# Optimization experiments

Hardware: AMD Instinct MI355X
Metric: run time of the kernel (lower is better)

## Reference

```python
import jax, jax.numpy as jnp
import numpy as np

B, S, D = 2, 2048, 1024
H = 16
DH = D // H  # 64


def setup_inputs() -> dict:
    key = jax.random.key(0)
    k1, k2, k3 = jax.random.split(key, 3)
    X = jax.random.normal(k1, (B, S, D), dtype=jnp.float32)
    # xavier_normal for Linear(D, 3*D): std = sqrt(2/(fan_in+fan_out))
    std_qkv = float(np.sqrt(2.0 / (D + 3 * D)))
    std_out = float(np.sqrt(2.0 / (D + D)))
    W_qkv = jax.random.normal(k2, (3 * H * DH, D), dtype=jnp.float32) * std_qkv
    W_out = jax.random.normal(k3, (D, H * DH), dtype=jnp.float32) * std_out
    return {"X": X, "W_qkv": W_qkv, "W_out": W_out}


def reference(X, W_qkv, W_out):
    b, s, d = X.shape
    # stacked projection: (b, s, 3*H*DH), then per-head chunk into q,k,v
    qkv = jnp.einsum('bsd,ed->bse', X, W_qkv)
    qkv = qkv.reshape(b, s, H, 3 * DH)
    q, k, v = jnp.split(qkv, 3, axis=-1)  # each (b, s, H, DH)
    scale = 1.0 / jnp.sqrt(jnp.asarray(DH, dtype=X.dtype))
    # naive unfused attention: full [b,H,s,s] score matrix
    scores = jnp.einsum('bqhd,bkhd->bhqk', q, k) * scale
    attn = jax.nn.softmax(scores, axis=-1)
    vals = jnp.einsum('bhqk,bkhd->bqhd', attn, v)
    vals = vals.reshape(b, s, H * DH)
    out = jnp.einsum('bse,de->bsd', vals, W_out)
    return out
```

## Files before the change

### kernel.cpp

```cpp
#include <hip/hip_runtime.h>
#include <cstdint>
#include <cstddef>

typedef __bf16 bf16;
typedef __bf16 bf16x8 __attribute__((ext_vector_type(8)));
typedef __bf16 bf16x2 __attribute__((ext_vector_type(2)));
typedef float  floatx4 __attribute__((ext_vector_type(4)));

typedef __attribute__((address_space(1))) void gvoid_t;
typedef __attribute__((address_space(3))) void lvoid_t;

#define MFMA16(a, b, c) __builtin_amdgcn_mfma_f32_16x16x32_bf16((a), (b), (c), 0, 0, 0)

#if __has_builtin(__builtin_amdgcn_exp2f)
#define EXP2(x) __builtin_amdgcn_exp2f(x)
#else
#define EXP2(x) exp2f(x)
#endif

#define S_TOK 2048
#define E3 3072
#define DMODEL 1024

#define NX 4194304
#define NWQ 3145728
#define NWO 1048576
__global__ __launch_bounds__(256) void cvt_all(const float* __restrict__ X,
                                               const float* __restrict__ Wq,
                                               const float* __restrict__ Wo,
                                               bf16* __restrict__ Xb,
                                               bf16* __restrict__ Wqb,
                                               bf16* __restrict__ Wob) {
  int i = (blockIdx.x * 256 + threadIdx.x) * 8;
  const float* s;
  bf16* d;
  float sc = 1.0f;
  int off;
  if (i < NX) {
    s = X; d = Xb; off = i;
  } else if (i < NX + NWQ) {
    off = i - NX; s = Wq; d = Wqb;
    int row = off >> 10;
    if ((row % 192) < 64) sc = 0.18033688011f;
  } else {
    off = i - NX - NWQ; s = Wo; d = Wob;
  }
  const float4* p = (const float4*)(s + off);
  float4 a = p[0], b = p[1];
  bf16x8 o;
  o[0] = (bf16)(a.x * sc); o[1] = (bf16)(a.y * sc);
  o[2] = (bf16)(a.z * sc); o[3] = (bf16)(a.w * sc);
  o[4] = (bf16)(b.x * sc); o[5] = (bf16)(b.y * sc);
  o[6] = (bf16)(b.z * sc); o[7] = (bf16)(b.w * sc);
  *(bf16x8*)(d + off) = o;
}

__device__ __forceinline__ void gl_lds16(const bf16* g, bf16* l) {
  __builtin_amdgcn_global_load_lds((gvoid_t*)g, (lvoid_t*)l, 16, 0, 0);
}

template <bool OUT_BF16>
__global__ __launch_bounds__(256) void gemm_bt(const bf16* __restrict__ A,
                                               const bf16* __restrict__ Bt,
                                               void* __restrict__ Cv,
                                               int M, int N, int K) {
  __shared__ bf16 sA[128 * 64];
  __shared__ bf16 sB[128 * 64];
  const int tid = threadIdx.x;
  const int wv = tid >> 6, lane = tid & 63;
  const int wr = wv >> 1, wc = wv & 1;
  const int lrow = lane & 15, lgrp = lane >> 4;
  const int R0 = blockIdx.y * 128, C0 = blockIdx.x * 128;

  floatx4 acc[4][4] = {};

  const int srow = lane >> 3;
  const int schk = (lane & 7) ^ srow;
  const bf16* gA = A + (size_t)(R0 + wv * 32 + srow) * K + schk * 8;
  const bf16* gB = Bt + (size_t)(C0 + wv * 32 + srow) * K + schk * 8;
  bf16* lA = sA + wv * 32 * 64;
  bf16* lB = sB + wv * 32 * 64;
  const size_t rs8 = (size_t)8 * K;

  for (int k0 = 0; k0 < K; k0 += 64) {
#pragma unroll
    for (int c = 0; c < 4; c++) {
      gl_lds16(gA + k0 + c * rs8, lA + c * 512);
      gl_lds16(gB + k0 + c * rs8, lB + c * 512);
    }
    __syncthreads();
#pragma unroll
    for (int kk = 0; kk < 2; kk++) {
      bf16x8 af[4], bfr[4];
#pragma unroll
      for (int i = 0; i < 4; i++) {
        int r = wr * 64 + i * 16 + lrow;
        af[i] = *(const bf16x8*)&sA[r * 64 + ((kk * 4 + lgrp) ^ (r & 7)) * 8];
      }
#pragma unroll
      for (int j = 0; j < 4; j++) {
        int r = wc * 64 + j * 16 + lrow;
        bfr[j] = *(const bf16x8*)&sB[r * 64 + ((kk * 4 + lgrp) ^ (r & 7)) * 8];
      }
#pragma unroll
      for (int i = 0; i < 4; i++)
#pragma unroll
        for (int j = 0; j < 4; j++)
          acc[i][j] = MFMA16(af[i], bfr[j], acc[i][j]);
    }
    __syncthreads();
  }

  const int rbase = R0 + wr * 64 + lgrp * 4;
  const int cbase = C0 + wc * 64 + lrow;
  if (OUT_BF16) {
    bf16* C = (bf16*)Cv;
#pragma unroll
    for (int i = 0; i < 4; i++)
#pragma unroll
      for (int j = 0; j < 4; j++)
#pragma unroll
        for (int r = 0; r < 4; r++)
          C[(size_t)(rbase + i * 16 + r) * N + cbase + j * 16] = (bf16)acc[i][j][r];
  } else {
    float* C = (float*)Cv;
#pragma unroll
    for (int i = 0; i < 4; i++)
#pragma unroll
      for (int j = 0; j < 4; j++)
#pragma unroll
        for (int r = 0; r < 4; r++)
          C[(size_t)(rbase + i * 16 + r) * N + cbase + j * 16] = acc[i][j][r];
  }
}

__global__ __launch_bounds__(256) void transpose_v(const bf16* __restrict__ qkv,
                                                   bf16* __restrict__ Vt) {
  __shared__ bf16 sT[64 * 72];
  const int tid = threadIdx.x;
  const int b = blockIdx.z, h = blockIdx.y, s0 = blockIdx.x * 64;
  const bf16* vsrc = qkv + (size_t)(b * S_TOK + s0) * E3 + h * 192 + 128;
#pragma unroll
  for (int j = 0; j < 8; j++) {
    int idx = tid + 256 * j;
    int sl = idx & 63, dp = idx >> 6;
    unsigned u = *(const unsigned*)(vsrc + (size_t)sl * E3 + 2 * dp);
    sT[(2 * dp) * 72 + sl] = __builtin_bit_cast(bf16, (unsigned short)(u & 0xffffu));
    sT[(2 * dp + 1) * 72 + sl] = __builtin_bit_cast(bf16, (unsigned short)(u >> 16));
  }
  __syncthreads();
  bf16* vdst = Vt + ((size_t)(b * 16 + h) * 64) * S_TOK + s0;
#pragma unroll
  for (int j = 0; j < 2; j++) {
    int idx = tid + 256 * j;
    int d = idx >> 3, sc8 = (idx & 7) * 8;
    bf16x8 o;
#pragma unroll
    for (int m2 = 0; m2 < 8; m2++) {
      int sp = sc8 + m2;
      int ss = (sp & ~31) | ((sp >> 1) & 15) | ((sp & 1) << 4);
      o[m2] = sT[d * 72 + ss];
    }
    *(bf16x8*)(vdst + (size_t)d * S_TOK + sc8) = o;
  }
}

__global__ __launch_bounds__(256, 3) void attn(const bf16* __restrict__ qkv,
                                               const bf16* __restrict__ Vt,
                                               bf16* __restrict__ vals) {
  __shared__ bf16 sK[2][64 * 64];
  __shared__ bf16 sV[2][64 * 64];
  __shared__ bf16 sP[4][2][16 * 40];

  const int tid = threadIdx.x;
  const int wv = tid >> 6, lane = tid & 63;
  const int lrow = lane & 15, lgrp = lane >> 4;
  const int b = blockIdx.z, h = blockIdx.y;
  const int qb = blockIdx.x * 128;

  const int srow = lane >> 3;
  const int scol = (lane & 7) ^ srow;
  const bf16* kg0 = qkv + (size_t)(b * S_TOK + wv * 16 + srow) * E3 + h * 192 + 64 + scol * 8;
  const bf16* vg0 = Vt + (size_t)((b * 16 + h) * 64 + wv * 16 + srow) * S_TOK + scol * 8;

  const bf16* qp = qkv + (size_t)(b * S_TOK + qb + wv * 32) * E3 + h * 192;
  bf16x8 qa[2][2];
#pragma unroll
  for (int rt = 0; rt < 2; rt++)
#pragma unroll
    for (int dh = 0; dh < 2; dh++)
      qa[rt][dh] = *(const bf16x8*)(qp + (size_t)(rt * 16 + lrow) * E3 + dh * 32 + lgrp * 8);

  floatx4 O[2][4] = {};
  floatx4 lacc[2] = {};
  bf16x8 ones;
  const bf16 one1 = (bf16)1.0f;
#pragma unroll
  for (int j = 0; j < 8; j++) ones[j] = one1;

  const int xsw = (lrow & 7);

  auto stage = [&](int buf, int kt) {
    const bf16* kg = kg0 + (size_t)kt * 64 * E3;
    gl_lds16(kg, &sK[buf][wv * 1024]);
    gl_lds16(kg + (size_t)8 * E3, &sK[buf][wv * 1024 + 512]);
    const bf16* vg = vg0 + kt * 64;
    gl_lds16(vg, &sV[buf][wv * 1024]);
    gl_lds16(vg + 8 * S_TOK, &sV[buf][wv * 1024 + 512]);
  };

  auto compute = [&](int buf) {
#pragma unroll
    for (int g = 0; g < 2; g++) {
      bf16x8 kf[2][2];
#pragma unroll
      for (int t = 0; t < 2; t++)
#pragma unroll
        for (int dh = 0; dh < 2; dh++)
          kf[t][dh] = *(const bf16x8*)&sK[buf][(g * 32 + t * 16 + lrow) * 64 +
                                              ((dh * 4 + lgrp) ^ xsw) * 8];
#pragma unroll
      for (int rt = 0; rt < 2; rt++) {
        floatx4 sc0 = {0.f, 0.f, 0.f, 0.f}, sc1 = {0.f, 0.f, 0.f, 0.f};
        sc0 = MFMA16(qa[rt][0], kf[0][0], sc0);
        sc0 = MFMA16(qa[rt][1], kf[0][1], sc0);
        sc1 = MFMA16(qa[rt][0], kf[1][0], sc1);
        sc1 = MFMA16(qa[rt][1], kf[1][1], sc1);
#pragma unroll
        for (int r = 0; r < 4; r++) {
          bf16x2 h2;
          h2[0] = (bf16)EXP2(sc0[r]);
          h2[1] = (bf16)EXP2(sc1[r]);
          *(unsigned*)&sP[wv][rt][(lgrp * 4 + r) * 40 + lrow * 2] =
              __builtin_bit_cast(unsigned, h2);
        }
      }
      bf16x8 vf[4];
#pragma unroll
      for (int dt = 0; dt < 4; dt++)
        vf[dt] = *(const bf16x8*)&sV[buf][(dt * 16 + lrow) * 64 +
                                          ((g * 4 + lgrp) ^ xsw) * 8];
#pragma unroll
      for (int rt = 0; rt < 2; rt++) {
        bf16x8 pf = *(const bf16x8*)&sP[wv][rt][lrow * 40 + lgrp * 8];
#pragma unroll
        for (int dt = 0; dt < 4; dt++) O[rt][dt] = MFMA16(pf, vf[dt], O[rt][dt]);
        lacc[rt] = MFMA16(pf, ones, lacc[rt]);
      }
    }
  };

  stage(0, 0);
  __syncthreads();
#pragma unroll 1
  for (int kt = 0; kt < 32; kt += 2) {
    stage(1, kt + 1);
    compute(0);
    __syncthreads();
    if (kt + 2 < 32) stage(0, kt + 2);
    compute(1);
    __syncthreads();
  }

  bf16* vout = vals + (size_t)(b * S_TOK + qb + wv * 32) * DMODEL + h * 64;
#pragma unroll
  for (int rt = 0; rt < 2; rt++)
#pragma unroll
    for (int r = 0; r < 4; r++) {
      float rinv = __builtin_amdgcn_rcpf(lacc[rt][r]);
#pragma unroll
      for (int dt = 0; dt < 4; dt++)
        vout[(size_t)(rt * 16 + lgrp * 4 + r) * DMODEL + dt * 16 + lrow] =
            (bf16)(O[rt][dt][r] * rinv);
    }
}

extern "C" void kernel_launch(void* const* d_in, const int* in_sizes, int n_in,
                              void* d_out, int out_size, void* d_ws, size_t ws_size,
                              hipStream_t stream) {
  const float* X = (const float*)d_in[0];
  const float* Wqkv = (const float*)d_in[1];
  const float* Wout = (const float*)d_in[2];
  float* out = (float*)d_out;

  char* ws = (char*)d_ws;
  bf16* Xb = (bf16*)(ws);
  bf16* Wqb = (bf16*)(ws + ((size_t)8 << 20));
  bf16* Wob = (bf16*)(ws + ((size_t)14 << 20));
  bf16* qkvb = (bf16*)(ws + ((size_t)16 << 20));
  bf16* Vt = (bf16*)(ws + ((size_t)40 << 20));
  bf16* vals = (bf16*)(ws + ((size_t)48 << 20));

  cvt_all<<<(NX + NWQ + NWO) / 2048, 256, 0, stream>>>(X, Wqkv, Wout, Xb, Wqb, Wob);

  gemm_bt<true><<<dim3(24, 32), 256, 0, stream>>>(Xb, Wqb, qkvb, 4096, 3072, 1024);

  transpose_v<<<dim3(32, 16, 2), 256, 0, stream>>>(qkvb, Vt);

  attn<<<dim3(16, 16, 2), 256, 0, stream>>>(qkvb, Vt, vals);

  gemm_bt<false><<<dim3(8, 32), 256, 0, stream>>>(vals, Wob, out, 4096, 1024, 1024);
}
```

Before: 186.9 us.

## Fuse V transpose into QKV GEMM epilogue, widen attention blocks, narrow output GEMM tiles

The QKV GEMM epilogue now writes the V columns straight into the transposed, permuted Vt layout, which removes the separate transpose_v kernel and its round trip through global memory. The attention kernel moves to 512 threads, with each wave handling 16 query rows instead of 32, which cuts per-wave registers and raises waves per block. The output projection gets a new 128x64-tile GEMM that launches twice as many blocks so the device is better filled. The cost is scattered 2-byte stores in the fused epilogue and less reuse of K/V data per wave in attention.

```diff
diff --git a/kernel.cpp b/kernel.cpp
--- a/kernel.cpp
+++ b/kernel.cpp
@@ -59,10 +59,11 @@
   __builtin_amdgcn_global_load_lds((gvoid_t*)g, (lvoid_t*)l, 16, 0, 0);
 }
 
-template <bool OUT_BF16>
+template <bool OUT_BF16, bool FUSE_V>
 __global__ __launch_bounds__(256) void gemm_bt(const bf16* __restrict__ A,
                                                const bf16* __restrict__ Bt,
                                                void* __restrict__ Cv,
+                                               bf16* __restrict__ Vt,
                                                int M, int N, int K) {
   __shared__ bf16 sA[128 * 64];
   __shared__ bf16 sB[128 * 64];
@@ -118,10 +119,25 @@
 #pragma unroll
     for (int i = 0; i < 4; i++)
 #pragma unroll
-      for (int j = 0; j < 4; j++)
-#pragma unroll
-        for (int r = 0; r < 4; r++)
-          C[(size_t)(rbase + i * 16 + r) * N + cbase + j * 16] = (bf16)acc[i][j][r];
+      for (int j = 0; j < 4; j++) {
+        const int col = cbase + j * 16;
+        const int m192 = col % 192;
+        const int hh = col / 192;
+#pragma unroll
+        for (int r = 0; r < 4; r++) {
+          const int row = rbase + i * 16 + r;
+          bf16 val = (bf16)acc[i][j][r];
+          bf16* dst;
+          if (FUSE_V && m192 >= 128) {
+            const int sl = row & 2047;
+            const int sp = (sl & ~31) | ((sl & 15) << 1) | ((sl >> 4) & 1);
+            dst = Vt + ((size_t)(((row >> 11) * 16 + hh) * 64 + (m192 - 128))) * S_TOK + sp;
+          } else {
+            dst = C + (size_t)row * N + col;
+          }
+          *dst = val;
+        }
+      }
   } else {
     float* C = (float*)Cv;
 #pragma unroll
@@ -134,43 +150,73 @@
   }
 }
 
-__global__ __launch_bounds__(256) void transpose_v(const bf16* __restrict__ qkv,
-                                                   bf16* __restrict__ Vt) {
-  __shared__ bf16 sT[64 * 72];
+__global__ __launch_bounds__(256) void gemm_bt_n64(const bf16* __restrict__ A,
+                                                   const bf16* __restrict__ Bt,
+                                                   float* __restrict__ C,
+                                                   int M, int N, int K) {
+  __shared__ bf16 sA[128 * 64];
+  __shared__ bf16 sB[64 * 64];
   const int tid = threadIdx.x;
-  const int b = blockIdx.z, h = blockIdx.y, s0 = blockIdx.x * 64;
-  const bf16* vsrc = qkv + (size_t)(b * S_TOK + s0) * E3 + h * 192 + 128;
-#pragma unroll
-  for (int j = 0; j < 8; j++) {
-    int idx = tid + 256 * j;
-    int sl = idx & 63, dp = idx >> 6;
-    unsigned u = *(const unsigned*)(vsrc + (size_t)sl * E3 + 2 * dp);
-    sT[(2 * dp) * 72 + sl] = __builtin_bit_cast(bf16, (unsigned short)(u & 0xffffu));
-    sT[(2 * dp + 1) * 72 + sl] = __builtin_bit_cast(bf16, (unsigned short)(u >> 16));
-  }
-  __syncthreads();
-  bf16* vdst = Vt + ((size_t)(b * 16 + h) * 64) * S_TOK + s0;
-#pragma unroll
-  for (int j = 0; j < 2; j++) {
-    int idx = tid + 256 * j;
-    int d = idx >> 3, sc8 = (idx & 7) * 8;
-    bf16x8 o;
-#pragma unroll
-    for (int m2 = 0; m2 < 8; m2++) {
-      int sp = sc8 + m2;
-      int ss = (sp & ~31) | ((sp >> 1) & 15) | ((sp & 1) << 4);
-      o[m2] = sT[d * 72 + ss];
+  const int wv = tid >> 6, lane = tid & 63;
+  const int wr = wv >> 1, wc = wv & 1;
+  const int lrow = lane & 15, lgrp = lane >> 4;
+  const int R0 = blockIdx.y * 128, C0 = blockIdx.x * 64;
+
+  floatx4 acc[4][2] = {};
+
+  const int srow = lane >> 3;
+  const int schk = (lane & 7) ^ srow;
+  const bf16* gA = A + (size_t)(R0 + wv * 32 + srow) * K + schk * 8;
+  const bf16* gB = Bt + (size_t)(C0 + wv * 16 + srow) * K + schk * 8;
+  bf16* lA = sA + wv * 32 * 64;
+  bf16* lB = sB + wv * 16 * 64;
+  const size_t rs8 = (size_t)8 * K;
+
+  for (int k0 = 0; k0 < K; k0 += 64) {
+#pragma unroll
+    for (int c = 0; c < 4; c++) gl_lds16(gA + k0 + c * rs8, lA + c * 512);
+#pragma unroll
+    for (int c = 0; c < 2; c++) gl_lds16(gB + k0 + c * rs8, lB + c * 512);
+    __syncthreads();
+#pragma unroll
+    for (int kk = 0; kk < 2; kk++) {
+      bf16x8 af[4], bfr[2];
+#pragma unroll
+      for (int i = 0; i < 4; i++) {
+        int r = wr * 64 + i * 16 + lrow;
+        af[i] = *(const bf16x8*)&sA[r * 64 + ((kk * 4 + lgrp) ^ (r & 7)) * 8];
+      }
+#pragma unroll
+      for (int j = 0; j < 2; j++) {
+        int r = wc * 32 + j * 16 + lrow;
+        bfr[j] = *(const bf16x8*)&sB[r * 64 + ((kk * 4 + lgrp) ^ (r & 7)) * 8];
+      }
+#pragma unroll
+      for (int i = 0; i < 4; i++)
+#pragma unroll
+        for (int j = 0; j < 2; j++)
+          acc[i][j] = MFMA16(af[i], bfr[j], acc[i][j]);
     }
-    *(bf16x8*)(vdst + (size_t)d * S_TOK + sc8) = o;
-  }
-}
-
-__global__ __launch_bounds__(256, 3) void attn(const bf16* __restrict__ qkv,
+    __syncthreads();
+  }
+
+  const int rbase = R0 + wr * 64 + lgrp * 4;
+  const int cbase = C0 + wc * 32 + lrow;
+#pragma unroll
+  for (int i = 0; i < 4; i++)
+#pragma unroll
+    for (int j = 0; j < 2; j++)
+#pragma unroll
+      for (int r = 0; r < 4; r++)
+        C[(size_t)(rbase + i * 16 + r) * N + cbase + j * 16] = acc[i][j][r];
+}
+
+__global__ __launch_bounds__(512, 4) void attn(const bf16* __restrict__ qkv,
                                                const bf16* __restrict__ Vt,
                                                bf16* __restrict__ vals) {
   __shared__ bf16 sK[2][64 * 64];
   __shared__ bf16 sV[2][64 * 64];
-  __shared__ bf16 sP[4][2][16 * 40];
+  __shared__ bf16 sP[8 * 640];
 
   const int tid = threadIdx.x;
   const int wv = tid >> 6, lane = tid & 63;
@@ -180,33 +226,28 @@
 
   const int srow = lane >> 3;
   const int scol = (lane & 7) ^ srow;
-  const bf16* kg0 = qkv + (size_t)(b * S_TOK + wv * 16 + srow) * E3 + h * 192 + 64 + scol * 8;
-  const bf16* vg0 = Vt + (size_t)((b * 16 + h) * 64 + wv * 16 + srow) * S_TOK + scol * 8;
-
-  const bf16* qp = qkv + (size_t)(b * S_TOK + qb + wv * 32) * E3 + h * 192;
-  bf16x8 qa[2][2];
-#pragma unroll
-  for (int rt = 0; rt < 2; rt++)
-#pragma unroll
-    for (int dh = 0; dh < 2; dh++)
-      qa[rt][dh] = *(const bf16x8*)(qp + (size_t)(rt * 16 + lrow) * E3 + dh * 32 + lgrp * 8);
-
-  floatx4 O[2][4] = {};
-  floatx4 lacc[2] = {};
+  const bf16* kg0 = qkv + (size_t)(b * S_TOK + wv * 8 + srow) * E3 + h * 192 + 64 + scol * 8;
+  const bf16* vg0 = Vt + (size_t)((b * 16 + h) * 64 + wv * 8 + srow) * S_TOK + scol * 8;
+
+  const bf16* qp = qkv + (size_t)(b * S_TOK + qb + wv * 16) * E3 + h * 192;
+  bf16x8 qa[2];
+#pragma unroll
+  for (int dh = 0; dh < 2; dh++)
+    qa[dh] = *(const bf16x8*)(qp + (size_t)lrow * E3 + dh * 32 + lgrp * 8);
+
+  floatx4 O[4] = {};
+  floatx4 lacc = {};
   bf16x8 ones;
   const bf16 one1 = (bf16)1.0f;
 #pragma unroll
   for (int j = 0; j < 8; j++) ones[j] = one1;
 
   const int xsw = (lrow & 7);
+  bf16* sPw = sP + wv * 640;
 
   auto stage = [&](int buf, int kt) {
-    const bf16* kg = kg0 + (size_t)kt * 64 * E3;
-    gl_lds16(kg, &sK[buf][wv * 1024]);
-    gl_lds16(kg + (size_t)8 * E3, &sK[buf][wv * 1024 + 512]);
-    const bf16* vg = vg0 + kt * 64;
-    gl_lds16(vg, &sV[buf][wv * 1024]);
-    gl_lds16(vg + 8 * S_TOK, &sV[buf][wv * 1024 + 512]);
+    gl_lds16(kg0 + (size_t)kt * 64 * E3, &sK[buf][wv * 512]);
+    gl_lds16(vg0 + kt * 64, &sV[buf][wv * 512]);
   };
 
   auto compute = [&](int buf) {
@@ -219,34 +260,28 @@
         for (int dh = 0; dh < 2; dh++)
           kf[t][dh] = *(const bf16x8*)&sK[buf][(g * 32 + t * 16 + lrow) * 64 +
                                               ((dh * 4 + lgrp) ^ xsw) * 8];
-#pragma unroll
-      for (int rt = 0; rt < 2; rt++) {
-        floatx4 sc0 = {0.f, 0.f, 0.f, 0.f}, sc1 = {0.f, 0.f, 0.f, 0.f};
-        sc0 = MFMA16(qa[rt][0], kf[0][0], sc0);
-        sc0 = MFMA16(qa[rt][1], kf[0][1], sc0);
-        sc1 = MFMA16(qa[rt][0], kf[1][0], sc1);
-        sc1 = MFMA16(qa[rt][1], kf[1][1], sc1);
-#pragma unroll
-        for (int r = 0; r < 4; r++) {
-          bf16x2 h2;
-          h2[0] = (bf16)EXP2(sc0[r]);
-          h2[1] = (bf16)EXP2(sc1[r]);
-          *(unsigned*)&sP[wv][rt][(lgrp * 4 + r) * 40 + lrow * 2] =
-              __builtin_bit_cast(unsigned, h2);
-        }
+      floatx4 sc0 = {0.f, 0.f, 0.f, 0.f}, sc1 = {0.f, 0.f, 0.f, 0.f};
+      sc0 = MFMA16(qa[0], kf[0][0], sc0);
+      sc0 = MFMA16(qa[1], kf[0][1], sc0);
+      sc1 = MFMA16(qa[0], kf[1][0], sc1);
+      sc1 = MFMA16(qa[1], kf[1][1], sc1);
+#pragma unroll
+      for (int r = 0; r < 4; r++) {
+        bf16x2 h2;
+        h2[0] = (bf16)EXP2(sc0[r]);
+        h2[1] = (bf16)EXP2(sc1[r]);
+        *(unsigned*)&sPw[(lgrp * 4 + r) * 40 + lrow * 2] =
+            __builtin_bit_cast(unsigned, h2);
       }
       bf16x8 vf[4];
 #pragma unroll
       for (int dt = 0; dt < 4; dt++)
         vf[dt] = *(const bf16x8*)&sV[buf][(dt * 16 + lrow) * 64 +
                                           ((g * 4 + lgrp) ^ xsw) * 8];
-#pragma unroll
-      for (int rt = 0; rt < 2; rt++) {
-        bf16x8 pf = *(const bf16x8*)&sP[wv][rt][lrow * 40 + lgrp * 8];
-#pragma unroll
-        for (int dt = 0; dt < 4; dt++) O[rt][dt] = MFMA16(pf, vf[dt], O[rt][dt]);
-        lacc[rt] = MFMA16(pf, ones, lacc[rt]);
-      }
+      bf16x8 pf = *(const bf16x8*)&sPw[lrow * 40 + lgrp * 8];
+#pragma unroll
+      for (int dt = 0; dt < 4; dt++) O[dt] = MFMA16(pf, vf[dt], O[dt]);
+      lacc = MFMA16(pf, ones, lacc);
     }
   };
 
@@ -262,17 +297,15 @@
     __syncthreads();
   }
 
-  bf16* vout = vals + (size_t)(b * S_TOK + qb + wv * 32) * DMODEL + h * 64;
-#pragma unroll
-  for (int rt = 0; rt < 2; rt++)
-#pragma unroll
-    for (int r = 0; r < 4; r++) {
-      float rinv = __builtin_amdgcn_rcpf(lacc[rt][r]);
-#pragma unroll
-      for (int dt = 0; dt < 4; dt++)
-        vout[(size_t)(rt * 16 + lgrp * 4 + r) * DMODEL + dt * 16 + lrow] =
-            (bf16)(O[rt][dt][r] * rinv);
-    }
+  bf16* vout = vals + (size_t)(b * S_TOK + qb + wv * 16) * DMODEL + h * 64;
+#pragma unroll
+  for (int r = 0; r < 4; r++) {
+    float rinv = __builtin_amdgcn_rcpf(lacc[r]);
+#pragma unroll
+    for (int dt = 0; dt < 4; dt++)
+      vout[(size_t)(lgrp * 4 + r) * DMODEL + dt * 16 + lrow] =
+          (bf16)(O[dt][r] * rinv);
+  }
 }
 
 extern "C" void kernel_launch(void* const* d_in, const int* in_sizes, int n_in,
@@ -293,11 +326,9 @@
 
   cvt_all<<<(NX + NWQ + NWO) / 2048, 256, 0, stream>>>(X, Wqkv, Wout, Xb, Wqb, Wob);
 
-  gemm_bt<true><<<dim3(24, 32), 256, 0, stream>>>(Xb, Wqb, qkvb, 4096, 3072, 1024);
-
-  transpose_v<<<dim3(32, 16, 2), 256, 0, stream>>>(qkvb, Vt);
-
-  attn<<<dim3(16, 16, 2), 256, 0, stream>>>(qkvb, Vt, vals);
-
-  gemm_bt<false><<<dim3(8, 32), 256, 0, stream>>>(vals, Wob, out, 4096, 1024, 1024);
-}
+  gemm_bt<true, true><<<dim3(24, 32), 256, 0, stream>>>(Xb, Wqb, qkvb, Vt, 4096, 3072, 1024);
+
+  attn<<<dim3(16, 16, 2), 512, 0, stream>>>(qkvb, Vt, vals);
+
+  gemm_bt_n64<<<dim3(16, 32), 256, 0, stream>>>(vals, Wob, out, 4096, 1024, 1024);
+}
```

New measurement: 180.0 us. 3.7% less time.
